# Performance work log

Measured on AMD Instinct MI355X. Metric: run time of the kernel, lower is better.

The kernel has to match this reference:

```python
import jax, jax.numpy as jnp
import numpy as np

TEMPERATURE = 0.5
EPS = 1e-12  # matches torch F.normalize default eps


def _l2_normalize(x):
    norm = jnp.sqrt(jnp.sum(x * x, axis=-1, keepdims=True))
    return x / jnp.maximum(norm, EPS)


def setup_inputs() -> dict:
    key = jax.random.key(0)
    k1, k2 = jax.random.split(key)
    B, C, D = 64, 512, 256
    visual_features = jax.random.normal(k1, (B, C, D), dtype=jnp.float32)
    text_embeddings = jax.random.normal(k2, (B, C, D), dtype=jnp.float32)
    return {"visual_features": visual_features, "text_embeddings": text_embeddings}


def reference(visual_features, text_embeddings):
    v = _l2_normalize(visual_features)   # (B, C, D)
    t = _l2_normalize(text_embeddings)   # (B, C, D)
    # positive: diagonal similarity per class
    sim_pos = jnp.einsum('bcd,bcd->bc', v, t)
    positive = jnp.exp(sim_pos / TEMPERATURE)            # (B, C)
    # full BxCxC similarity matrix
    all_sim = jnp.exp(jnp.einsum('bcd,bkd->bck', v, t) / TEMPERATURE)
    negative = jnp.sum(all_sim, axis=-1) - positive      # (B, C)
    loss = -jnp.log(positive / (positive + negative))
    return jnp.mean(loss)
```

## Files before the change

kernel.cpp:

```cpp
#include <hip/hip_runtime.h>
#include <hip/hip_bf16.h>

#define BB 64
#define CC 512
#define DD 256

typedef __attribute__((ext_vector_type(8))) short bf16x8;
typedef __attribute__((ext_vector_type(4))) float f32x4;
typedef unsigned int u32;

#define SWZ(r) (((r) & 7) << 4)

__device__ inline short f2bf(float f) {
    union { __hip_bfloat16 h; short s; } cv;
    cv.h = __float2bfloat16(f);
    return cv.s;
}

__global__ __launch_bounds__(256) void norm_rows(const float* __restrict__ in,
                                                 unsigned short* __restrict__ out) {
    const int row  = blockIdx.x * 4 + (threadIdx.x >> 6);
    const int lane = threadIdx.x & 63;
    const float4 x = reinterpret_cast<const float4*>(in)[(size_t)row * 64 + lane];
    float ss = x.x * x.x + x.y * x.y + x.z * x.z + x.w * x.w;
#pragma unroll
    for (int off = 32; off; off >>= 1) ss += __shfl_xor(ss, off);
    const float r = 1.0f / fmaxf(sqrtf(ss), 1e-12f);
    ushort4 o;
    o.x = (unsigned short)f2bf(x.x * r);
    o.y = (unsigned short)f2bf(x.y * r);
    o.z = (unsigned short)f2bf(x.z * r);
    o.w = (unsigned short)f2bf(x.w * r);
    reinterpret_cast<ushort4*>(out)[(size_t)row * 64 + lane] = o;
}

__global__ __launch_bounds__(512, 1) void gemm_loss(const float* __restrict__ V,
                                                    const unsigned short* __restrict__ Tn,
                                                    float* __restrict__ partials) {
    extern __shared__ char lds[];
    float* vred = reinterpret_cast<float*>(lds + 131072);
    float* dred = vred + 256;
    float* red2 = dred + 256;

    const int i0    = blockIdx.x;
    const int inner = i0 & 63;
    const int b     = (inner & 7) * 8 + (inner >> 3);
    const int rb    = i0 >> 6;

    const int tid  = threadIdx.x;
    const int lane = tid & 63;
    const int wave = tid >> 6;
    const int wr   = wave >> 1;
    const int wc   = wave & 1;
    const int g    = lane >> 4;
    const int ln   = lane & 15;

    const float* gV = V + (size_t)b * (CC * DD) + (size_t)rb * 128 * DD;
    const char*  gT = reinterpret_cast<const char*>(Tn + (size_t)b * (CC * DD));

    {
        const int rrow  = tid >> 3;
        const int ecolB = (tid & 7) * 64;
#pragma unroll
        for (int p = 0; p < 2; ++p) {
            const int row = p * 64 + rrow;
            const float4* src =
                reinterpret_cast<const float4*>(gV + (size_t)row * DD) + (tid & 7) * 8;
            float4 x[8];
#pragma unroll
            for (int q = 0; q < 8; ++q) x[q] = src[q];
            float ss = 0.f;
#pragma unroll
            for (int q = 0; q < 8; ++q)
                ss += x[q].x * x[q].x + x[q].y * x[q].y + x[q].z * x[q].z + x[q].w * x[q].w;
            ss += __shfl_xor(ss, 1);
            ss += __shfl_xor(ss, 2);
            ss += __shfl_xor(ss, 4);
            const float rinv = 1.0f / fmaxf(sqrtf(ss), 1e-12f);
            char* dstrow = lds + row * 512;
            const int sw = SWZ(row);
#pragma unroll
            for (int q2 = 0; q2 < 4; ++q2) {
                const float4 v0 = x[2 * q2], v1 = x[2 * q2 + 1];
                bf16x8 o;
                o[0] = f2bf(v0.x * rinv); o[1] = f2bf(v0.y * rinv);
                o[2] = f2bf(v0.z * rinv); o[3] = f2bf(v0.w * rinv);
                o[4] = f2bf(v1.x * rinv); o[5] = f2bf(v1.y * rinv);
                o[6] = f2bf(v1.z * rinv); o[7] = f2bf(v1.w * rinv);
                *reinterpret_cast<bf16x8*>(dstrow + ((ecolB + q2 * 16) ^ sw)) = o;
            }
        }
    }
    __syncthreads();

    bf16x8 a[2][8];
#pragma unroll
    for (int i = 0; i < 2; ++i) {
        const int row  = wr * 32 + i * 16 + ln;
        const char* rp = lds + row * 512;
        const int sw   = SWZ(row);
#pragma unroll
        for (int kk = 0; kk < 8; ++kk)
            a[i][kk] = *reinterpret_cast<const bf16x8*>(rp + ((kk * 64 + g * 16) ^ sw));
    }
    __syncthreads();

    auto stage = [&](int t) {
        const char* gtile = gT + (size_t)t * 32768;
        char* dst = lds + (t & 3) * 32768 + wave * 4096;
#pragma unroll
        for (int r2 = 0; r2 < 4; ++r2) {
            const int L   = r2 * 1024 + (lane << 4);
            const int lr  = L >> 9;
            const int row = wave * 8 + lr;
            const int inrow = L & 511;
            __builtin_amdgcn_global_load_lds(
                (const u32*)(gtile + (size_t)row * 512 + (inrow ^ SWZ(row))),
                (u32*)(dst + r2 * 1024), 16, 0, 0);
        }
    };
    stage(0);
    stage(1);
    stage(2);

    float rs[2][4];
    float dg[2][4];
#pragma unroll
    for (int i = 0; i < 2; ++i)
#pragma unroll
        for (int r = 0; r < 4; ++r) { rs[i][r] = 0.f; dg[i][r] = 0.f; }

    for (int t = 0; t < 8; ++t) {
        if (t < 6)      asm volatile("s_waitcnt vmcnt(8)" ::: "memory");
        else if (t == 6) asm volatile("s_waitcnt vmcnt(4)" ::: "memory");
        else            asm volatile("s_waitcnt vmcnt(0)" ::: "memory");
        __builtin_amdgcn_s_barrier();
        __builtin_amdgcn_sched_barrier(0);
        if (t < 5) stage(t + 3);

        const char* bufp = lds + (t & 3) * 32768;
        const int row0 = wc * 32 + ln;
        const int row1 = wc * 32 + 16 + ln;
        const char* rp0 = bufp + row0 * 512;
        const char* rp1 = bufp + row1 * 512;
        const int sw0 = SWZ(row0), sw1 = SWZ(row1);
        f32x4 acc[2][2];
#pragma unroll
        for (int i = 0; i < 2; ++i)
#pragma unroll
            for (int j = 0; j < 2; ++j) acc[i][j] = (f32x4){0.f, 0.f, 0.f, 0.f};
        __builtin_amdgcn_s_setprio(1);
#pragma unroll
        for (int kk = 0; kk < 8; ++kk) {
            const int ko = kk * 64 + g * 16;
            const bf16x8 b0 = *reinterpret_cast<const bf16x8*>(rp0 + (ko ^ sw0));
            const bf16x8 b1 = *reinterpret_cast<const bf16x8*>(rp1 + (ko ^ sw1));
            acc[0][0] = __builtin_amdgcn_mfma_f32_16x16x32_bf16(a[0][kk], b0, acc[0][0], 0, 0, 0);
            acc[1][0] = __builtin_amdgcn_mfma_f32_16x16x32_bf16(a[1][kk], b0, acc[1][0], 0, 0, 0);
            acc[0][1] = __builtin_amdgcn_mfma_f32_16x16x32_bf16(a[0][kk], b1, acc[0][1], 0, 0, 0);
            acc[1][1] = __builtin_amdgcn_mfma_f32_16x16x32_bf16(a[1][kk], b1, acc[1][1], 0, 0, 0);
        }
        __builtin_amdgcn_s_setprio(0);

        if ((t >> 1) == rb) {
#pragma unroll
            for (int i = 0; i < 2; ++i) {
                const int grow = rb * 128 + wr * 32 + i * 16 + g * 4;
#pragma unroll
                for (int j = 0; j < 2; ++j) {
                    const int gcol = t * 64 + wc * 32 + j * 16 + ln;
#pragma unroll
                    for (int r = 0; r < 4; ++r) {
                        const float s2 = acc[i][j][r] * 2.0f;
                        rs[i][r] += __expf(s2);
                        if (gcol == grow + r) dg[i][r] += s2;
                    }
                }
            }
        } else {
#pragma unroll
            for (int i = 0; i < 2; ++i)
#pragma unroll
                for (int j = 0; j < 2; ++j)
#pragma unroll
                    for (int r = 0; r < 4; ++r) rs[i][r] += __expf(acc[i][j][r] * 2.0f);
        }
    }

#pragma unroll
    for (int i = 0; i < 2; ++i)
#pragma unroll
        for (int r = 0; r < 4; ++r) {
            float v = rs[i][r];
            float d = dg[i][r];
#pragma unroll
            for (int m = 1; m < 16; m <<= 1) {
                v += __shfl_xor(v, m);
                d += __shfl_xor(d, m);
            }
            if (ln == 0) {
                const int rl = wr * 32 + i * 16 + g * 4 + r;
                vred[rl * 2 + wc] = v;
                dred[rl * 2 + wc] = d;
            }
        }
    __syncthreads();

    if (tid < 128) {
        const float vv = vred[tid * 2] + vred[tid * 2 + 1];
        const float dd = dred[tid * 2] + dred[tid * 2 + 1];
        float lsum = logf(vv) - dd;
#pragma unroll
        for (int m = 1; m < 64; m <<= 1) lsum += __shfl_xor(lsum, m);
        if (lane == 0) red2[wave] = lsum;
    }
    __syncthreads();
    if (tid == 0) partials[i0] = red2[0] + red2[1];
}

__global__ __launch_bounds__(256) void final_reduce(const float* __restrict__ partials,
                                                    float* __restrict__ out) {
    const int t = threadIdx.x;
    float v = partials[t];
#pragma unroll
    for (int m = 1; m < 64; m <<= 1) v += __shfl_xor(v, m);
    __shared__ float red[4];
    if ((t & 63) == 0) red[t >> 6] = v;
    __syncthreads();
    if (t == 0) out[0] = (red[0] + red[1] + red[2] + red[3]) * (1.0f / 32768.0f);
}

extern "C" void kernel_launch(void* const* d_in, const int* in_sizes, int n_in,
                              void* d_out, int out_size, void* d_ws, size_t ws_size,
                              hipStream_t stream) {
    const float* vis = (const float*)d_in[0];
    const float* txt = (const float*)d_in[1];

    unsigned short* Tn = (unsigned short*)d_ws;
    float* partials    = (float*)((char*)d_ws + (size_t)BB * CC * DD * 2);
    float* out         = (float*)d_out;

    const int lds_bytes = 131072 + 256 * 4 + 256 * 4 + 16;
    hipFuncSetAttribute((const void*)gemm_loss, hipFuncAttributeMaxDynamicSharedMemorySize,
                        lds_bytes);

    norm_rows<<<8192, 256, 0, stream>>>(txt, Tn);
    gemm_loss<<<256, 512, lds_bytes, stream>>>(vis, Tn, partials);
    final_reduce<<<1, 256, 0, stream>>>(partials, out);
}
```

Baseline: 35.50 us.

## Fuse text-row normalization into GEMM loss kernel and drop the separate pass

Removes the standalone norm_rows kernel that wrote a normalized bf16 copy of the text embeddings. Each GEMM block now makes a first pass over its batch's fp32 text rows to compute the reciprocal norms into LDS. It then streams the fp32 tiles through registers with double buffering, scaling and converting them to bf16 in LDS. This is meant to save a kernel launch and the global write and re-read of the intermediate tensor. In exchange, each block reads the fp32 text data twice, and the four blocks sharing a batch each redo it, which raises cache and HBM traffic. The async global-to-LDS 4-stage pipeline is also replaced by a simpler register prefetch with block barriers.

```diff
diff --git a/kernel.cpp b/kernel.cpp
--- a/kernel.cpp
+++ b/kernel.cpp
@@ -7,7 +7,6 @@
 
 typedef __attribute__((ext_vector_type(8))) short bf16x8;
 typedef __attribute__((ext_vector_type(4))) float f32x4;
-typedef unsigned int u32;
 
 #define SWZ(r) (((r) & 7) << 4)
 
@@ -17,28 +16,12 @@
     return cv.s;
 }
 
-__global__ __launch_bounds__(256) void norm_rows(const float* __restrict__ in,
-                                                 unsigned short* __restrict__ out) {
-    const int row  = blockIdx.x * 4 + (threadIdx.x >> 6);
-    const int lane = threadIdx.x & 63;
-    const float4 x = reinterpret_cast<const float4*>(in)[(size_t)row * 64 + lane];
-    float ss = x.x * x.x + x.y * x.y + x.z * x.z + x.w * x.w;
-#pragma unroll
-    for (int off = 32; off; off >>= 1) ss += __shfl_xor(ss, off);
-    const float r = 1.0f / fmaxf(sqrtf(ss), 1e-12f);
-    ushort4 o;
-    o.x = (unsigned short)f2bf(x.x * r);
-    o.y = (unsigned short)f2bf(x.y * r);
-    o.z = (unsigned short)f2bf(x.z * r);
-    o.w = (unsigned short)f2bf(x.w * r);
-    reinterpret_cast<ushort4*>(out)[(size_t)row * 64 + lane] = o;
-}
-
 __global__ __launch_bounds__(512, 1) void gemm_loss(const float* __restrict__ V,
-                                                    const unsigned short* __restrict__ Tn,
+                                                    const float* __restrict__ T,
                                                     float* __restrict__ partials) {
     extern __shared__ char lds[];
-    float* vred = reinterpret_cast<float*>(lds + 131072);
+    float* rcpn = reinterpret_cast<float*>(lds + 65536);
+    float* vred = reinterpret_cast<float*>(lds + 65536 + 2048);
     float* dred = vred + 256;
     float* red2 = dred + 256;
 
@@ -55,40 +38,54 @@
     const int g    = lane >> 4;
     const int ln   = lane & 15;
 
-    const float* gV = V + (size_t)b * (CC * DD) + (size_t)rb * 128 * DD;
-    const char*  gT = reinterpret_cast<const char*>(Tn + (size_t)b * (CC * DD));
-
-    {
-        const int rrow  = tid >> 3;
-        const int ecolB = (tid & 7) * 64;
-#pragma unroll
-        for (int p = 0; p < 2; ++p) {
-            const int row = p * 64 + rrow;
-            const float4* src =
-                reinterpret_cast<const float4*>(gV + (size_t)row * DD) + (tid & 7) * 8;
-            float4 x[8];
-#pragma unroll
-            for (int q = 0; q < 8; ++q) x[q] = src[q];
-            float ss = 0.f;
-#pragma unroll
-            for (int q = 0; q < 8; ++q)
-                ss += x[q].x * x[q].x + x[q].y * x[q].y + x[q].z * x[q].z + x[q].w * x[q].w;
-            ss += __shfl_xor(ss, 1);
-            ss += __shfl_xor(ss, 2);
-            ss += __shfl_xor(ss, 4);
-            const float rinv = 1.0f / fmaxf(sqrtf(ss), 1e-12f);
-            char* dstrow = lds + row * 512;
-            const int sw = SWZ(row);
-#pragma unroll
-            for (int q2 = 0; q2 < 4; ++q2) {
-                const float4 v0 = x[2 * q2], v1 = x[2 * q2 + 1];
-                bf16x8 o;
-                o[0] = f2bf(v0.x * rinv); o[1] = f2bf(v0.y * rinv);
-                o[2] = f2bf(v0.z * rinv); o[3] = f2bf(v0.w * rinv);
-                o[4] = f2bf(v1.x * rinv); o[5] = f2bf(v1.y * rinv);
-                o[6] = f2bf(v1.z * rinv); o[7] = f2bf(v1.w * rinv);
-                *reinterpret_cast<bf16x8*>(dstrow + ((ecolB + q2 * 16) ^ sw)) = o;
-            }
+    const float* gV  = V + (size_t)b * (CC * DD) + (size_t)rb * 128 * DD;
+    const float* gT  = T + (size_t)b * (CC * DD);
+
+    const int rrow  = tid >> 3;
+    const int ecolB = (tid & 7) * 64;
+
+#pragma unroll
+    for (int p = 0; p < 8; ++p) {
+        const int row = p * 64 + rrow;
+        const float4* src = reinterpret_cast<const float4*>(gT + (size_t)row * DD) + (tid & 7) * 8;
+        float ss = 0.f;
+#pragma unroll
+        for (int q = 0; q < 8; ++q) {
+            const float4 xq = src[q];
+            ss += xq.x * xq.x + xq.y * xq.y + xq.z * xq.z + xq.w * xq.w;
+        }
+        ss += __shfl_xor(ss, 1);
+        ss += __shfl_xor(ss, 2);
+        ss += __shfl_xor(ss, 4);
+        if ((tid & 7) == 0) rcpn[row] = 1.0f / fmaxf(sqrtf(ss), 1e-12f);
+    }
+
+#pragma unroll
+    for (int p = 0; p < 2; ++p) {
+        const int row = p * 64 + rrow;
+        const float4* src = reinterpret_cast<const float4*>(gV + (size_t)row * DD) + (tid & 7) * 8;
+        float4 x[8];
+#pragma unroll
+        for (int q = 0; q < 8; ++q) x[q] = src[q];
+        float ss = 0.f;
+#pragma unroll
+        for (int q = 0; q < 8; ++q)
+            ss += x[q].x * x[q].x + x[q].y * x[q].y + x[q].z * x[q].z + x[q].w * x[q].w;
+        ss += __shfl_xor(ss, 1);
+        ss += __shfl_xor(ss, 2);
+        ss += __shfl_xor(ss, 4);
+        const float rinv = 1.0f / fmaxf(sqrtf(ss), 1e-12f);
+        char* dstrow = lds + row * 512;
+        const int sw = SWZ(row);
+#pragma unroll
+        for (int q2 = 0; q2 < 4; ++q2) {
+            const float4 v0 = x[2 * q2], v1 = x[2 * q2 + 1];
+            bf16x8 o;
+            o[0] = f2bf(v0.x * rinv); o[1] = f2bf(v0.y * rinv);
+            o[2] = f2bf(v0.z * rinv); o[3] = f2bf(v0.w * rinv);
+            o[4] = f2bf(v1.x * rinv); o[5] = f2bf(v1.y * rinv);
+            o[6] = f2bf(v1.z * rinv); o[7] = f2bf(v1.w * rinv);
+            *reinterpret_cast<bf16x8*>(dstrow + ((ecolB + q2 * 16) ^ sw)) = o;
         }
     }
     __syncthreads();
@@ -105,23 +102,32 @@
     }
     __syncthreads();
 
-    auto stage = [&](int t) {
-        const char* gtile = gT + (size_t)t * 32768;
-        char* dst = lds + (t & 3) * 32768 + wave * 4096;
-#pragma unroll
-        for (int r2 = 0; r2 < 4; ++r2) {
-            const int L   = r2 * 1024 + (lane << 4);
-            const int lr  = L >> 9;
-            const int row = wave * 8 + lr;
-            const int inrow = L & 511;
-            __builtin_amdgcn_global_load_lds(
-                (const u32*)(gtile + (size_t)row * 512 + (inrow ^ SWZ(row))),
-                (u32*)(dst + r2 * 1024), 16, 0, 0);
-        }
+    float4 x[8];
+    auto t_load = [&](int tt) {
+        const float4* src =
+            reinterpret_cast<const float4*>(gT + (size_t)(tt * 64 + rrow) * DD) + (tid & 7) * 8;
+#pragma unroll
+        for (int q = 0; q < 8; ++q) x[q] = src[q];
     };
-    stage(0);
-    stage(1);
-    stage(2);
+    auto t_write = [&](int tt) {
+        const float sc = rcpn[tt * 64 + rrow];
+        char* dstrow   = lds + (tt & 1) * 32768 + rrow * 512;
+        const int sw   = SWZ(rrow);
+#pragma unroll
+        for (int q2 = 0; q2 < 4; ++q2) {
+            const float4 v0 = x[2 * q2], v1 = x[2 * q2 + 1];
+            bf16x8 o;
+            o[0] = f2bf(v0.x * sc); o[1] = f2bf(v0.y * sc);
+            o[2] = f2bf(v0.z * sc); o[3] = f2bf(v0.w * sc);
+            o[4] = f2bf(v1.x * sc); o[5] = f2bf(v1.y * sc);
+            o[6] = f2bf(v1.z * sc); o[7] = f2bf(v1.w * sc);
+            *reinterpret_cast<bf16x8*>(dstrow + ((ecolB + q2 * 16) ^ sw)) = o;
+        }
+    };
+
+    t_load(0);
+    t_write(0);
+    __syncthreads();
 
     float rs[2][4];
     float dg[2][4];
@@ -131,14 +137,9 @@
         for (int r = 0; r < 4; ++r) { rs[i][r] = 0.f; dg[i][r] = 0.f; }
 
     for (int t = 0; t < 8; ++t) {
-        if (t < 6)      asm volatile("s_waitcnt vmcnt(8)" ::: "memory");
-        else if (t == 6) asm volatile("s_waitcnt vmcnt(4)" ::: "memory");
-        else            asm volatile("s_waitcnt vmcnt(0)" ::: "memory");
-        __builtin_amdgcn_s_barrier();
-        __builtin_amdgcn_sched_barrier(0);
-        if (t < 5) stage(t + 3);
-
-        const char* bufp = lds + (t & 3) * 32768;
+        if (t < 7) t_load(t + 1);
+
+        const char* bufp = lds + (t & 1) * 32768;
         const int row0 = wc * 32 + ln;
         const int row1 = wc * 32 + 16 + ln;
         const char* rp0 = bufp + row0 * 512;
@@ -185,6 +186,9 @@
 #pragma unroll
                     for (int r = 0; r < 4; ++r) rs[i][r] += __expf(acc[i][j][r] * 2.0f);
         }
+
+        if (t < 7) t_write(t + 1);
+        __syncthreads();
     }
 
 #pragma unroll
@@ -236,15 +240,13 @@
     const float* vis = (const float*)d_in[0];
     const float* txt = (const float*)d_in[1];
 
-    unsigned short* Tn = (unsigned short*)d_ws;
-    float* partials    = (float*)((char*)d_ws + (size_t)BB * CC * DD * 2);
-    float* out         = (float*)d_out;
-
-    const int lds_bytes = 131072 + 256 * 4 + 256 * 4 + 16;
+    float* partials = (float*)d_ws;
+    float* out      = (float*)d_out;
+
+    const int lds_bytes = 65536 + 2048 + 1024 + 1024 + 16;
     hipFuncSetAttribute((const void*)gemm_loss, hipFuncAttributeMaxDynamicSharedMemorySize,
                         lds_bytes);
 
-    norm_rows<<<8192, 256, 0, stream>>>(txt, Tn);
-    gemm_loss<<<256, 512, lds_bytes, stream>>>(vis, Tn, partials);
+    gemm_loss<<<256, 512, lds_bytes, stream>>>(vis, txt, partials);
     final_reduce<<<1, 256, 0, stream>>>(partials, out);
 }
```

Result: slower. 47.64 us (+34.2%).
